# Optimization experiments

Hardware: AMD Instinct MI355X
Metric: run time of the kernel (lower is better)

The kernel has to match this reference:

```python
import jax, jax.numpy as jnp
import numpy as np

THEA = 0.5
DELTA = 1.5
IGNORE = 255
K = 19  # num classes (len(weights))
LOSS_WEIGHT = 1.0
MIN_PIXELS = 20.0  # class kept only if pixel count > 20
WEIGHTS = jnp.ones((K,), dtype=jnp.float32)
EPS = 1e-12


def setup_inputs() -> dict:
    key = jax.random.key(0)
    k1, k2 = jax.random.split(key)
    n, c, h, w = 4, 32, 512, 1024
    predict = jax.random.normal(k1, (n, c, h, w), dtype=jnp.float32)
    target = jax.random.randint(k2, (n, h, w), 0, K, dtype=jnp.int32)
    return {"predict": predict, "target": target}


def _loss(predict, target):
    n, c, h, w = predict.shape
    # (n,c,h,w) -> (n*h*w, c), matching predict.permute(0,2,3,1)
    feat = jnp.transpose(predict, (0, 2, 3, 1)).reshape(-1, c)
    seg = target.reshape(-1)
    valid_pix = seg != IGNORE
    seg = jnp.where(valid_pix, seg, K).astype(jnp.int32)  # ignored -> extra segment K
    ones = valid_pix.astype(feat.dtype)

    # per-class counts and means (segment reduce replaces the python class loop)
    counts = jax.ops.segment_sum(ones, seg, num_segments=K + 1)[:K]
    sums = jax.ops.segment_sum(feat * ones[:, None], seg, num_segments=K + 1)[:K]
    centers = sums / jnp.maximum(counts, 1.0)[:, None]  # [K, c]
    valid_cls = counts > MIN_PIXELS
    n_cls = jnp.maximum(jnp.sum(valid_cls.astype(feat.dtype)), 1.0)

    # ---- variance term: relu(||mean - x|| - thea)^2, normalized by #positives ----
    ctr_ext = jnp.concatenate([centers, jnp.zeros((1, c), centers.dtype)], axis=0)
    ctr_pix = ctr_ext[seg]  # gather per-pixel center
    res = jnp.sqrt(jnp.sum((ctr_pix - feat) ** 2, axis=1) + EPS)  # [n*h*w]
    r = jax.nn.relu(res - THEA) * ones
    sq = jax.ops.segment_sum(r * r, seg, num_segments=K + 1)[:K]
    pos = jax.ops.segment_sum((r > 0).astype(feat.dtype), seg, num_segments=K + 1)[:K]
    norml = jnp.maximum(jax.lax.stop_gradient(pos), 1.0)  # numpy count in original: no grad
    loss_var = jnp.sum(jnp.where(valid_cls, WEIGHTS * sq / norml, 0.0)) / n_cls

    # ---- pairwise center distance term ----
    diff = centers[:, None, :] - centers[None, :, :]  # [K, K, c]
    dist = jnp.sqrt(jnp.sum(diff * diff, axis=-1) + EPS)
    pair_mask = valid_cls[:, None] & valid_cls[None, :] & ~jnp.eye(K, dtype=bool)
    d = jax.nn.relu(2.0 * DELTA - dist)
    loss_dis = jnp.sum(jnp.where(pair_mask, d * d, 0.0)) / jnp.maximum(n_cls * (n_cls - 1.0), 1.0)

    # ---- regularization term ----
    loss_reg = jnp.sum(jnp.where(valid_cls, jnp.sqrt(jnp.sum(centers * centers, axis=1) + EPS), 0.0)) / n_cls

    return LOSS_WEIGHT * (loss_var + loss_dis + 0.001 * loss_reg)


def reference(predict, target):
    return _loss(predict, target)
```

## Files before the change

### kernel.cpp

```cpp
#include <hip/hip_runtime.h>


#define K_CLS 19
#define C_CH 32
#define HW_SHIFT 19
#define HW_SIZE (1 << HW_SHIFT)
#define EPSF 1e-12f
#define THEA_F 0.5f
#define TWO_DELTA 3.0f
#define MIN_PIX 20.0f

#define OFF_PSUM 0
#define OFF_PCNT 40960
#define OFF_RED  42240
#define OFF_VRED 42880
#define OFF_VPART 42944
#define WS_FLOATS (OFF_VPART + 1024 * 64)

typedef const unsigned int __attribute__((address_space(1)))* GP;
typedef unsigned int __attribute__((address_space(3)))* LP;

__device__ __forceinline__ void atomAddF(float* p, float v) {
  unsafeAtomicAdd(p, v);
}

__global__ __launch_bounds__(256) void k_accum(
    const float* __restrict__ pred, const int* __restrict__ tgt,
    float* __restrict__ ws)
{
  __shared__ float sA[4][K_CLS][64];
  __shared__ float sB[4][K_CLS][64];
  __shared__ float s_w[4][20];
  const int t = threadIdx.x;
  const int w = t >> 6;
  const int lane = t & 63;
  float* colA = &sA[w][0][lane];
  float* colB = &sB[w][0][lane];
#pragma unroll
  for (int k = 0; k < K_CLS; ++k) { colA[k << 6] = 0.f; colB[k << 6] = 0.f; }

  if (blockIdx.x < 2048) {
    const int plane = blockIdx.x >> 4;
    const int slab  = blockIdx.x & 15;
    const int n_idx = plane >> 5;
    const int ch    = plane & 31;
    const float* pbase = pred + (((size_t)plane) << HW_SHIFT) + ((size_t)slab << 15);
    const int*   tbase = tgt  + (((size_t)n_idx) << HW_SHIFT) + ((size_t)slab << 15);

    float4 vA = *reinterpret_cast<const float4*>(pbase + t * 4);
    int4   cA = *reinterpret_cast<const int4*>(tbase + t * 4);
#pragma unroll 1
    for (int it = 0; it < 32; ++it) {
      float4 vB; int4 cB;
      if (it + 1 < 32) {
        vB = *reinterpret_cast<const float4*>(pbase + (it + 1) * 1024 + t * 4);
        cB = *reinterpret_cast<const int4*>(tbase + (it + 1) * 1024 + t * 4);
      }
      const float x[4] = {vA.x, vA.y, vA.z, vA.w};
      const int   s[4] = {cA.x, cA.y, cA.z, cA.w};
      const int   k0 = min((unsigned)s[0], 18u), k1 = min((unsigned)s[1], 18u);
      const int   k2 = min((unsigned)s[2], 18u), k3 = min((unsigned)s[3], 18u);
      const float v0 = ((unsigned)s[0] < K_CLS) ? x[0] : 0.f;
      const float v1 = ((unsigned)s[1] < K_CLS) ? x[1] : 0.f;
      const float v2 = ((unsigned)s[2] < K_CLS) ? x[2] : 0.f;
      const float v3 = ((unsigned)s[3] < K_CLS) ? x[3] : 0.f;
      colA[k0 << 6] += v0;
      colB[k1 << 6] += v1;
      colA[k2 << 6] += v2;
      colB[k3 << 6] += v3;
      vA = vB; cA = cB;
    }

    float acc[K_CLS];
#pragma unroll
    for (int k = 0; k < K_CLS; ++k) acc[k] = colA[k << 6] + colB[k << 6];
#pragma unroll
    for (int k = 0; k < K_CLS; ++k) {
      float s = acc[k];
#pragma unroll
      for (int m = 1; m < 64; m <<= 1) s += __shfl_xor(s, m, 64);
      acc[k] = s;
    }
#pragma unroll
    for (int k = 0; k < K_CLS; ++k)
      if (lane == k) s_w[w][k] = acc[k];
    __syncthreads();
    if (t < K_CLS) {
      const int slot = n_idx * 16 + slab;
      ws[OFF_PSUM + ch * (64 * 20) + slot * 20 + t] =
          s_w[0][t] + s_w[1][t] + s_w[2][t] + s_w[3][t];
    }
  } else {
    const int idx = blockIdx.x - 2048;
    const int n_idx = idx >> 4;
    const int slab  = idx & 15;
    const int* tbase = tgt + (((size_t)n_idx) << HW_SHIFT) + ((size_t)slab << 15);

#pragma unroll 1
    for (int it = 0; it < 32; ++it) {
      const int4 c4 = *reinterpret_cast<const int4*>(tbase + it * 1024 + t * 4);
      const int s[4] = {c4.x, c4.y, c4.z, c4.w};
      const int k0 = min((unsigned)s[0], 18u), k1 = min((unsigned)s[1], 18u);
      const int k2 = min((unsigned)s[2], 18u), k3 = min((unsigned)s[3], 18u);
      colA[k0 << 6] += ((unsigned)s[0] < K_CLS) ? 1.f : 0.f;
      colB[k1 << 6] += ((unsigned)s[1] < K_CLS) ? 1.f : 0.f;
      colA[k2 << 6] += ((unsigned)s[2] < K_CLS) ? 1.f : 0.f;
      colB[k3 << 6] += ((unsigned)s[3] < K_CLS) ? 1.f : 0.f;
    }

    float acc[K_CLS];
#pragma unroll
    for (int k = 0; k < K_CLS; ++k) acc[k] = colA[k << 6] + colB[k << 6];
#pragma unroll
    for (int k = 0; k < K_CLS; ++k) {
      float s = acc[k];
#pragma unroll
      for (int m = 1; m < 64; m <<= 1) s += __shfl_xor(s, m, 64);
      acc[k] = s;
    }
#pragma unroll
    for (int k = 0; k < K_CLS; ++k)
      if (lane == k) s_w[w][k] = acc[k];
    __syncthreads();
    if (t < K_CLS) {
      const int slot = n_idx * 16 + slab;
      ws[OFF_PCNT + slot * 20 + t] = s_w[0][t] + s_w[1][t] + s_w[2][t] + s_w[3][t];
    }
  }
}

__global__ __launch_bounds__(64) void k_reduce(float* __restrict__ ws)
{
  const int o = blockIdx.x;
  const int lane = threadIdx.x;
  float a;
  if (o < C_CH * K_CLS) {
    const int ch = o / K_CLS, k = o - ch * K_CLS;
    a = ws[OFF_PSUM + ch * (64 * 20) + lane * 20 + k];
  } else {
    a = ws[OFF_PCNT + lane * 20 + (o - C_CH * K_CLS)];
  }
#pragma unroll
  for (int m = 1; m < 64; m <<= 1) a += __shfl_xor(a, m, 64);
  if (lane == 0) ws[OFF_RED + o] = a;
}

__global__ __launch_bounds__(256) void k_var(
    const float* __restrict__ pred, const int* __restrict__ tgt,
    float* __restrict__ ws)
{
  __shared__ float s_buf[4][2][C_CH][64];
  __shared__ int   s_cls[4][2][256];
  __shared__ float s_ctr[C_CH][K_CLS];
  __shared__ float s_sq[K_CLS];
  __shared__ float s_pos[K_CLS];

  const int t = threadIdx.x;
  const int w = t >> 6;
  const int lane = t & 63;

  for (int i = t; i < C_CH * K_CLS; i += 256) {
    const int k = i % K_CLS;
    (&s_ctr[0][0])[i] = ws[OFF_RED + i] / fmaxf(ws[OFF_RED + C_CH * K_CLS + k], 1.f);
  }
  if (t < K_CLS) { s_sq[t] = 0.f; s_pos[t] = 0.f; }
  __syncthreads();

  const size_t P0 = (size_t)blockIdx.x * 2048;
  const int n_idx = (int)(P0 >> HW_SHIFT);
  const int hw0 = (int)(P0 & (HW_SIZE - 1));
  const int qch = lane >> 4;
  const int qpx = (lane & 15) * 4;

#define STAGE(h, j)                                                           \
  {                                                                           \
    const int pw = hw0 + w * 512 + (j) * 64;                                  \
    _Pragma("unroll")                                                         \
    for (int q = 0; q < 8; ++q) {                                             \
      const int c = q * 4 + qch;                                              \
      const float* gp = pred + (((size_t)(n_idx * C_CH + c)) << HW_SHIFT)     \
                        + pw + qpx;                                           \
      __builtin_amdgcn_global_load_lds((GP)gp, (LP)&s_buf[w][h][0][0] + q * 256, \
                                       16, 0, 0);                             \
    }                                                                         \
    const int* gt = tgt + (((size_t)n_idx) << HW_SHIFT) + pw + qpx;           \
    __builtin_amdgcn_global_load_lds((GP)gt, (LP)&s_cls[w][h][0], 16, 0, 0);  \
  }

  float res8[8];
  int   cls8[8];

  STAGE(0, 0)
#pragma unroll 1
  for (int j = 0; j < 8; ++j) {
    const int h = j & 1;
    if (j < 7) {
      STAGE(h ^ 1, j + 1)
      asm volatile("s_waitcnt vmcnt(9)" ::: "memory");
    } else {
      asm volatile("s_waitcnt vmcnt(0)" ::: "memory");
    }
    __builtin_amdgcn_sched_barrier(0);

    const int ci = s_cls[w][h][lane];
    const bool vld = (unsigned)ci < K_CLS;
    const int sc = vld ? ci : 0;
    float d2 = 0.f;
#pragma unroll
    for (int c = 0; c < C_CH; ++c) {
      const float x = s_buf[w][h][c][lane];
      const float d = s_ctr[c][sc] - x;
      d2 = fmaf(d, d, d2);
    }
    res8[j] = d2;
    cls8[j] = vld ? ci : -1;
  }

#pragma unroll
  for (int j = 0; j < 8; ++j) {
    if (cls8[j] >= 0) {
      const float r = sqrtf(res8[j] + EPSF) - THEA_F;
      if (r > 0.f) { atomAddF(&s_sq[cls8[j]], r * r); atomAddF(&s_pos[cls8[j]], 1.f); }
    }
  }

  __syncthreads();
  if (t < K_CLS) {
    float* vp = ws + OFF_VPART + (size_t)blockIdx.x * 64;
    vp[t]         = s_sq[t];
    vp[K_CLS + t] = s_pos[t];
  }
#undef STAGE
}

__global__ __launch_bounds__(256) void k_vred(float* __restrict__ ws)
{
  const int o = blockIdx.x;
  const int t = threadIdx.x;
  float a = 0.f;
#pragma unroll
  for (int r = 0; r < 4; ++r)
    a += ws[OFF_VPART + (size_t)(t + r * 256) * 64 + o];
#pragma unroll
  for (int m = 1; m < 64; m <<= 1) a += __shfl_xor(a, m, 64);
  __shared__ float s[4];
  if ((t & 63) == 0) s[t >> 6] = a;
  __syncthreads();
  if (t == 0) ws[OFF_VRED + o] = s[0] + s[1] + s[2] + s[3];
}

__global__ __launch_bounds__(1024) void k_final(
    float* __restrict__ ws, float* __restrict__ out)
{
  __shared__ float s_ctr[C_CH * K_CLS];
  __shared__ float s_valid[K_CLS];
  __shared__ float s_red[3];
  __shared__ float s_ncls;
  const int t = threadIdx.x;
  if (t < 3) s_red[t] = 0.f;
  if (t < K_CLS) s_valid[t] = (ws[OFF_RED + C_CH * K_CLS + t] > MIN_PIX) ? 1.f : 0.f;
  for (int i = t; i < C_CH * K_CLS; i += 1024) {
    const int k = i % K_CLS;
    s_ctr[i] = ws[OFF_RED + i] / fmaxf(ws[OFF_RED + C_CH * K_CLS + k], 1.f);
  }
  __syncthreads();

  if (t == 0) {
    float n = 0.f;
    for (int k = 0; k < K_CLS; ++k) n += s_valid[k];
    s_ncls = fmaxf(n, 1.f);
  }
  if (t < K_CLS && s_valid[t] > 0.f) {
    const float sq  = ws[OFF_VRED + t];
    const float pos = ws[OFF_VRED + K_CLS + t];
    atomAddF(&s_red[0], sq / fmaxf(pos, 1.f));
    float nn = 0.f;
#pragma unroll
    for (int ch = 0; ch < C_CH; ++ch) {
      const float cv = s_ctr[ch * K_CLS + t];
      nn = fmaf(cv, cv, nn);
    }
    atomAddF(&s_red[2], sqrtf(nn + EPSF));
  }
  if (t < K_CLS * K_CLS) {
    const int a = t / K_CLS, b = t - (t / K_CLS) * K_CLS;
    if (a != b && s_valid[a] > 0.f && s_valid[b] > 0.f) {
      float dd = 0.f;
#pragma unroll
      for (int ch = 0; ch < C_CH; ++ch) {
        const float df = s_ctr[ch * K_CLS + a] - s_ctr[ch * K_CLS + b];
        dd = fmaf(df, df, dd);
      }
      const float dist = sqrtf(dd + EPSF);
      const float d = fmaxf(TWO_DELTA - dist, 0.f);
      if (d > 0.f) atomAddF(&s_red[1], d * d);
    }
  }
  __syncthreads();
  if (t == 0) {
    const float n = s_ncls;
    out[0] = s_red[0] / n
           + s_red[1] / fmaxf(n * (n - 1.f), 1.f)
           + 0.001f * s_red[2] / n;
  }
}

extern "C" void kernel_launch(void* const* d_in, const int* in_sizes, int n_in,
                              void* d_out, int out_size, void* d_ws, size_t ws_size,
                              hipStream_t stream) {
  const float* pred = (const float*)d_in[0];
  const int*   tgt  = (const int*)d_in[1];
  float* ws  = (float*)d_ws;
  float* out = (float*)d_out;
  const int P = in_sizes[1];
  const int nBlocksVar = P / 2048;

  k_accum <<<2048 + 64, 256, 0, stream>>>(pred, tgt, ws);
  k_reduce<<<C_CH * K_CLS + K_CLS, 64, 0, stream>>>(ws);
  k_var   <<<nBlocksVar, 256, 0, stream>>>(pred, tgt, ws);
  k_vred  <<<2 * K_CLS, 256, 0, stream>>>(ws);
  k_final <<<1, 1024, 0, stream>>>(ws, out);
}
```

Before: 449.6 us.

## Shrink LDS staging in variance kernel and replace shared atomics with register accumulators

The variance kernel now stages 16 channels per half-stage instead of 32, cutting its LDS footprint roughly in half so more blocks can be resident per CU. The wait counts are adjusted to match. Per-class sums and positive counts are kept in per-lane register arrays with select-based updates and reduced by wave shuffles, replacing shared-memory atomics. The accumulation kernel also drops its second per-class column buffer, accepting more LDS read-modify-write dependency in exchange for less LDS. The extra register arrays and the 19-way select per pixel add ALU work and register pressure.

```diff
diff --git a/kernel.cpp b/kernel.cpp
--- a/kernel.cpp
+++ b/kernel.cpp
@@ -29,15 +29,13 @@
     float* __restrict__ ws)
 {
   __shared__ float sA[4][K_CLS][64];
-  __shared__ float sB[4][K_CLS][64];
   __shared__ float s_w[4][20];
   const int t = threadIdx.x;
   const int w = t >> 6;
   const int lane = t & 63;
   float* colA = &sA[w][0][lane];
-  float* colB = &sB[w][0][lane];
-#pragma unroll
-  for (int k = 0; k < K_CLS; ++k) { colA[k << 6] = 0.f; colB[k << 6] = 0.f; }
+#pragma unroll
+  for (int k = 0; k < K_CLS; ++k) colA[k << 6] = 0.f;
 
   if (blockIdx.x < 2048) {
     const int plane = blockIdx.x >> 4;
@@ -65,15 +63,15 @@
       const float v2 = ((unsigned)s[2] < K_CLS) ? x[2] : 0.f;
       const float v3 = ((unsigned)s[3] < K_CLS) ? x[3] : 0.f;
       colA[k0 << 6] += v0;
-      colB[k1 << 6] += v1;
+      colA[k1 << 6] += v1;
       colA[k2 << 6] += v2;
-      colB[k3 << 6] += v3;
+      colA[k3 << 6] += v3;
       vA = vB; cA = cB;
     }
 
     float acc[K_CLS];
 #pragma unroll
-    for (int k = 0; k < K_CLS; ++k) acc[k] = colA[k << 6] + colB[k << 6];
+    for (int k = 0; k < K_CLS; ++k) acc[k] = colA[k << 6];
 #pragma unroll
     for (int k = 0; k < K_CLS; ++k) {
       float s = acc[k];
@@ -103,14 +101,14 @@
       const int k0 = min((unsigned)s[0], 18u), k1 = min((unsigned)s[1], 18u);
       const int k2 = min((unsigned)s[2], 18u), k3 = min((unsigned)s[3], 18u);
       colA[k0 << 6] += ((unsigned)s[0] < K_CLS) ? 1.f : 0.f;
-      colB[k1 << 6] += ((unsigned)s[1] < K_CLS) ? 1.f : 0.f;
+      colA[k1 << 6] += ((unsigned)s[1] < K_CLS) ? 1.f : 0.f;
       colA[k2 << 6] += ((unsigned)s[2] < K_CLS) ? 1.f : 0.f;
-      colB[k3 << 6] += ((unsigned)s[3] < K_CLS) ? 1.f : 0.f;
+      colA[k3 << 6] += ((unsigned)s[3] < K_CLS) ? 1.f : 0.f;
     }
 
     float acc[K_CLS];
 #pragma unroll
-    for (int k = 0; k < K_CLS; ++k) acc[k] = colA[k << 6] + colB[k << 6];
+    for (int k = 0; k < K_CLS; ++k) acc[k] = colA[k << 6];
 #pragma unroll
     for (int k = 0; k < K_CLS; ++k) {
       float s = acc[k];
@@ -149,11 +147,10 @@
     const float* __restrict__ pred, const int* __restrict__ tgt,
     float* __restrict__ ws)
 {
-  __shared__ float s_buf[4][2][C_CH][64];
-  __shared__ int   s_cls[4][2][256];
+  __shared__ float s_buf[4][2][16][64];
+  __shared__ int   s_cls[4][2][64];
   __shared__ float s_ctr[C_CH][K_CLS];
-  __shared__ float s_sq[K_CLS];
-  __shared__ float s_pos[K_CLS];
+  __shared__ float s_w[4][40];
 
   const int t = threadIdx.x;
   const int w = t >> 6;
@@ -163,74 +160,99 @@
     const int k = i % K_CLS;
     (&s_ctr[0][0])[i] = ws[OFF_RED + i] / fmaxf(ws[OFF_RED + C_CH * K_CLS + k], 1.f);
   }
-  if (t < K_CLS) { s_sq[t] = 0.f; s_pos[t] = 0.f; }
   __syncthreads();
 
   const size_t P0 = (size_t)blockIdx.x * 2048;
   const int n_idx = (int)(P0 >> HW_SHIFT);
   const int hw0 = (int)(P0 & (HW_SIZE - 1));
-  const int qch = lane >> 4;
-  const int qpx = (lane & 15) * 4;
-
-#define STAGE(h, j)                                                           \
+
+#define VSTAGE(s_)                                                            \
   {                                                                           \
-    const int pw = hw0 + w * 512 + (j) * 64;                                  \
+    const int p_ = (s_) & 1, pxw_ = (s_) >> 1;                                \
+    const int pw_ = hw0 + w * 512 + pxw_ * 64;                                \
+    const int cb_ = p_ * 16;                                                  \
     _Pragma("unroll")                                                         \
-    for (int q = 0; q < 8; ++q) {                                             \
-      const int c = q * 4 + qch;                                              \
-      const float* gp = pred + (((size_t)(n_idx * C_CH + c)) << HW_SHIFT)     \
-                        + pw + qpx;                                           \
-      __builtin_amdgcn_global_load_lds((GP)gp, (LP)&s_buf[w][h][0][0] + q * 256, \
+    for (int q = 0; q < 4; ++q) {                                             \
+      const int ch_ = cb_ + q * 4 + (lane >> 4);                              \
+      const float* gp = pred + (((size_t)(n_idx * C_CH + ch_)) << HW_SHIFT)   \
+                        + pw_ + (lane & 15) * 4;                              \
+      __builtin_amdgcn_global_load_lds((GP)gp, (LP)&s_buf[w][p_][q * 4][0],   \
                                        16, 0, 0);                             \
     }                                                                         \
-    const int* gt = tgt + (((size_t)n_idx) << HW_SHIFT) + pw + qpx;           \
-    __builtin_amdgcn_global_load_lds((GP)gt, (LP)&s_cls[w][h][0], 16, 0, 0);  \
-  }
-
-  float res8[8];
-  int   cls8[8];
-
-  STAGE(0, 0)
+    if (p_ == 0 && lane < 16) {                                               \
+      const int* gt = tgt + (((size_t)n_idx) << HW_SHIFT) + pw_ + lane * 4;   \
+      __builtin_amdgcn_global_load_lds((GP)gt, (LP)&s_cls[w][pxw_ & 1][0],    \
+                                       16, 0, 0);                             \
+    }                                                                         \
+  }
+
+  float acc_sq[K_CLS], acc_pos[K_CLS];
+#pragma unroll
+  for (int k = 0; k < K_CLS; ++k) { acc_sq[k] = 0.f; acc_pos[k] = 0.f; }
+
+  int  ci = 0, sc = 0;
+  bool vld = false;
+  float d2 = 0.f;
+
+  VSTAGE(0)
 #pragma unroll 1
-  for (int j = 0; j < 8; ++j) {
-    const int h = j & 1;
-    if (j < 7) {
-      STAGE(h ^ 1, j + 1)
-      asm volatile("s_waitcnt vmcnt(9)" ::: "memory");
+  for (int s = 0; s < 16; ++s) {
+    if (s < 15) {
+      VSTAGE(s + 1)
+      if (s & 1) asm volatile("s_waitcnt vmcnt(5)" ::: "memory");
+      else       asm volatile("s_waitcnt vmcnt(4)" ::: "memory");
     } else {
       asm volatile("s_waitcnt vmcnt(0)" ::: "memory");
     }
     __builtin_amdgcn_sched_barrier(0);
 
-    const int ci = s_cls[w][h][lane];
-    const bool vld = (unsigned)ci < K_CLS;
-    const int sc = vld ? ci : 0;
-    float d2 = 0.f;
-#pragma unroll
-    for (int c = 0; c < C_CH; ++c) {
-      const float x = s_buf[w][h][c][lane];
-      const float d = s_ctr[c][sc] - x;
+    const int p = s & 1, pxw = s >> 1, cb = p * 16;
+    if (p == 0) {
+      ci = s_cls[w][pxw & 1][lane];
+      vld = (unsigned)ci < K_CLS;
+      sc = vld ? ci : 0;
+      d2 = 0.f;
+    }
+#pragma unroll
+    for (int cc = 0; cc < 16; ++cc) {
+      const float x = s_buf[w][p][cc][lane];
+      const float d = s_ctr[cb + cc][sc] - x;
       d2 = fmaf(d, d, d2);
     }
-    res8[j] = d2;
-    cls8[j] = vld ? ci : -1;
-  }
-
-#pragma unroll
-  for (int j = 0; j < 8; ++j) {
-    if (cls8[j] >= 0) {
-      const float r = sqrtf(res8[j] + EPSF) - THEA_F;
-      if (r > 0.f) { atomAddF(&s_sq[cls8[j]], r * r); atomAddF(&s_pos[cls8[j]], 1.f); }
-    }
-  }
-
+    if (p == 1) {
+      const float r = sqrtf(d2 + EPSF) - THEA_F;
+      const bool act = vld && (r > 0.f);
+      const float rr = act ? r * r : 0.f;
+      const float pp = act ? 1.f : 0.f;
+#pragma unroll
+      for (int k = 0; k < K_CLS; ++k) {
+        const bool b = (sc == k);
+        acc_sq[k]  += b ? rr : 0.f;
+        acc_pos[k] += b ? pp : 0.f;
+      }
+    }
+  }
+#undef VSTAGE
+
+#pragma unroll
+  for (int k = 0; k < K_CLS; ++k) {
+    float a = acc_sq[k], b = acc_pos[k];
+#pragma unroll
+    for (int m = 1; m < 64; m <<= 1) {
+      a += __shfl_xor(a, m, 64);
+      b += __shfl_xor(b, m, 64);
+    }
+    acc_sq[k] = a; acc_pos[k] = b;
+  }
+#pragma unroll
+  for (int k = 0; k < K_CLS; ++k)
+    if (lane == k) { s_w[w][k] = acc_sq[k]; s_w[w][20 + k] = acc_pos[k]; }
   __syncthreads();
   if (t < K_CLS) {
     float* vp = ws + OFF_VPART + (size_t)blockIdx.x * 64;
-    vp[t]         = s_sq[t];
-    vp[K_CLS + t] = s_pos[t];
-  }
-#undef STAGE
+    vp[t]         = s_w[0][t] + s_w[1][t] + s_w[2][t] + s_w[3][t];
+    vp[K_CLS + t] = s_w[0][20 + t] + s_w[1][20 + t] + s_w[2][20 + t] + s_w[3][20 + t];
+  }
 }
 
 __global__ __launch_bounds__(256) void k_vred(float* __restrict__ ws)
```

New measurement: 436.0 us. 3.0% less time.

## Fuse accumulate, reduce and variance passes into one persistent kernel with grid barriers

Applied to the files above, without the earlier changes.

Merges the per-class sum/count accumulation, the partial reduction and the variance pass into a single 512-block kernel of 512 threads, synchronised by software grid barriers on a workspace counter that is cleared with a memset before launch. Counts are now computed inside the accumulation blocks instead of in separate blocks, and the variance pass uses a 3-slot async LDS ring with transposed center storage and vectorised center reads. The intent is to remove launch gaps and tail effects between the former kernels. In exchange it relies on all 512 blocks being co-resident, since the spin barrier deadlocks otherwise, and it uses fewer, larger blocks.

```diff
diff --git a/kernel.cpp b/kernel.cpp
--- a/kernel.cpp
+++ b/kernel.cpp
@@ -4,18 +4,18 @@
 #define K_CLS 19
 #define C_CH 32
 #define HW_SHIFT 19
-#define HW_SIZE (1 << HW_SHIFT)
 #define EPSF 1e-12f
 #define THEA_F 0.5f
 #define TWO_DELTA 3.0f
 #define MIN_PIX 20.0f
+#define NBLK 512
 
 #define OFF_PSUM 0
-#define OFF_PCNT 40960
-#define OFF_RED  42240
-#define OFF_VRED 42880
-#define OFF_VPART 42944
-#define WS_FLOATS (OFF_VPART + 1024 * 64)
+#define OFF_PCNT 10240
+#define OFF_RED  20480
+#define OFF_VRED 21120
+#define OFF_VPART 21184
+#define OFF_BAR  53952
 
 typedef const unsigned int __attribute__((address_space(1)))* GP;
 typedef unsigned int __attribute__((address_space(3)))* LP;
@@ -24,46 +24,99 @@
   unsafeAtomicAdd(p, v);
 }
 
-__global__ __launch_bounds__(256) void k_accum(
+#define SMEM_BYTES 78464
+
+__device__ __forceinline__ void grid_barrier(unsigned* bar, int phase) {
+  __syncthreads();
+  if (threadIdx.x == 0) {
+    __threadfence();
+    __hip_atomic_fetch_add(&bar[phase * 16 + (blockIdx.x & 15)], 1u,
+                           __ATOMIC_RELEASE, __HIP_MEMORY_SCOPE_AGENT);
+    unsigned sum = 0;
+    do {
+      __builtin_amdgcn_s_sleep(8);
+      sum = 0;
+      for (int i = 0; i < 16; ++i)
+        sum += __hip_atomic_load(&bar[phase * 16 + i],
+                                 __ATOMIC_ACQUIRE, __HIP_MEMORY_SCOPE_AGENT);
+    } while (sum < NBLK);
+  }
+  __syncthreads();
+}
+
+__global__ __launch_bounds__(512, 4) void k_fused(
     const float* __restrict__ pred, const int* __restrict__ tgt,
-    float* __restrict__ ws)
+    float* __restrict__ ws, unsigned* __restrict__ bar)
 {
-  __shared__ float sA[4][K_CLS][64];
-  __shared__ float sB[4][K_CLS][64];
-  __shared__ float s_w[4][20];
+  __shared__ __align__(16) char smem[SMEM_BYTES];
+  float* smf = (float*)smem;
   const int t = threadIdx.x;
   const int w = t >> 6;
   const int lane = t & 63;
-  float* colA = &sA[w][0][lane];
-  float* colB = &sB[w][0][lane];
-#pragma unroll
-  for (int k = 0; k < K_CLS; ++k) { colA[k << 6] = 0.f; colB[k << 6] = 0.f; }
-
-  if (blockIdx.x < 2048) {
-    const int plane = blockIdx.x >> 4;
-    const int slab  = blockIdx.x & 15;
+  const int bid = blockIdx.x;
+
+  {
+    const int plane = bid >> 2;
+    const int slab  = bid & 3;
     const int n_idx = plane >> 5;
     const int ch    = plane & 31;
-    const float* pbase = pred + (((size_t)plane) << HW_SHIFT) + ((size_t)slab << 15);
-    const int*   tbase = tgt  + (((size_t)n_idx) << HW_SHIFT) + ((size_t)slab << 15);
+    const float* pbase = pred + (((size_t)plane) << HW_SHIFT) + ((size_t)slab << 17);
+    const int*   tbase = tgt  + (((size_t)n_idx) << HW_SHIFT) + ((size_t)slab << 17);
+
+    float* colA = smf + w * (K_CLS * 64) + lane;
+    float* colB = smf + 9728 + w * (K_CLS * 64) + lane;
+#pragma unroll
+    for (int k = 0; k < K_CLS; ++k) { colA[k << 6] = 0.f; colB[k << 6] = 0.f; }
+
+    {
+      const int* cb = tbase + ch * 4096;
+      const int4 c0 = *reinterpret_cast<const int4*>(cb + t * 8);
+      const int4 c1 = *reinterpret_cast<const int4*>(cb + t * 8 + 4);
+      const int cs[8] = {c0.x, c0.y, c0.z, c0.w, c1.x, c1.y, c1.z, c1.w};
+      float accc[K_CLS];
+#pragma unroll
+      for (int k = 0; k < K_CLS; ++k) accc[k] = 0.f;
+#pragma unroll
+      for (int j = 0; j < 8; ++j) {
+#pragma unroll
+        for (int k = 0; k < K_CLS; ++k) accc[k] += (cs[j] == k) ? 1.f : 0.f;
+      }
+#pragma unroll
+      for (int k = 0; k < K_CLS; ++k) {
+        float s = accc[k];
+#pragma unroll
+        for (int m = 1; m < 64; m <<= 1) s += __shfl_xor(s, m, 64);
+        accc[k] = s;
+      }
+      float* s_w = smf + 19456;
+#pragma unroll
+      for (int k = 0; k < K_CLS; ++k)
+        if (lane == k) s_w[w * 20 + k] = accc[k];
+      __syncthreads();
+      if (t < K_CLS) {
+        float a = 0.f;
+#pragma unroll
+        for (int ww = 0; ww < 8; ++ww) a += s_w[ww * 20 + t];
+        ws[OFF_PCNT + bid * 20 + t] = a;
+      }
+      __syncthreads();
+    }
 
     float4 vA = *reinterpret_cast<const float4*>(pbase + t * 4);
     int4   cA = *reinterpret_cast<const int4*>(tbase + t * 4);
 #pragma unroll 1
-    for (int it = 0; it < 32; ++it) {
+    for (int it = 0; it < 64; ++it) {
       float4 vB; int4 cB;
-      if (it + 1 < 32) {
-        vB = *reinterpret_cast<const float4*>(pbase + (it + 1) * 1024 + t * 4);
-        cB = *reinterpret_cast<const int4*>(tbase + (it + 1) * 1024 + t * 4);
-      }
-      const float x[4] = {vA.x, vA.y, vA.z, vA.w};
-      const int   s[4] = {cA.x, cA.y, cA.z, cA.w};
-      const int   k0 = min((unsigned)s[0], 18u), k1 = min((unsigned)s[1], 18u);
-      const int   k2 = min((unsigned)s[2], 18u), k3 = min((unsigned)s[3], 18u);
-      const float v0 = ((unsigned)s[0] < K_CLS) ? x[0] : 0.f;
-      const float v1 = ((unsigned)s[1] < K_CLS) ? x[1] : 0.f;
-      const float v2 = ((unsigned)s[2] < K_CLS) ? x[2] : 0.f;
-      const float v3 = ((unsigned)s[3] < K_CLS) ? x[3] : 0.f;
+      if (it + 1 < 64) {
+        vB = *reinterpret_cast<const float4*>(pbase + (it + 1) * 2048 + t * 4);
+        cB = *reinterpret_cast<const int4*>(tbase + (it + 1) * 2048 + t * 4);
+      }
+      const int k0 = min((unsigned)cA.x, 18u), k1 = min((unsigned)cA.y, 18u);
+      const int k2 = min((unsigned)cA.z, 18u), k3 = min((unsigned)cA.w, 18u);
+      const float v0 = ((unsigned)cA.x < K_CLS) ? vA.x : 0.f;
+      const float v1 = ((unsigned)cA.y < K_CLS) ? vA.y : 0.f;
+      const float v2 = ((unsigned)cA.z < K_CLS) ? vA.z : 0.f;
+      const float v3 = ((unsigned)cA.w < K_CLS) ? vA.w : 0.f;
       colA[k0 << 6] += v0;
       colB[k1 << 6] += v1;
       colA[k2 << 6] += v2;
@@ -81,156 +134,141 @@
       for (int m = 1; m < 64; m <<= 1) s += __shfl_xor(s, m, 64);
       acc[k] = s;
     }
-#pragma unroll
-    for (int k = 0; k < K_CLS; ++k)
-      if (lane == k) s_w[w][k] = acc[k];
+    {
+      float* s_w = smf + 19456;
+#pragma unroll
+      for (int k = 0; k < K_CLS; ++k)
+        if (lane == k) s_w[w * 20 + k] = acc[k];
+      __syncthreads();
+      if (t < K_CLS) {
+        float a = 0.f;
+#pragma unroll
+        for (int ww = 0; ww < 8; ++ww) a += s_w[ww * 20 + t];
+        ws[OFF_PSUM + ch * 320 + (n_idx * 4 + slab) * 20 + t] = a;
+      }
+    }
+  }
+
+  grid_barrier(bar, 0);
+
+  {
+    const int ch = bid / K_CLS, k = bid - ch * K_CLS;
+    if (t < 16) {
+      float a = ws[OFF_PSUM + ch * 320 + t * 20 + k];
+      a += __shfl_xor(a, 1, 64);
+      a += __shfl_xor(a, 2, 64);
+      a += __shfl_xor(a, 4, 64);
+      a += __shfl_xor(a, 8, 64);
+      if (t == 0) ws[OFF_RED + bid] = a;
+    }
+  }
+  if (bid < 96) {
+    const int j = bid + 512;
+    const int ch = j / K_CLS, k = j - ch * K_CLS;
+    if (t < 16) {
+      float a = ws[OFF_PSUM + ch * 320 + t * 20 + k];
+      a += __shfl_xor(a, 1, 64);
+      a += __shfl_xor(a, 2, 64);
+      a += __shfl_xor(a, 4, 64);
+      a += __shfl_xor(a, 8, 64);
+      if (t == 0) ws[OFF_RED + j] = a;
+    }
+  } else if (bid < 99) {
+    const int k = (bid - 96) * 8 + w;
+    if (k < K_CLS) {
+      float a = 0.f;
+#pragma unroll
+      for (int m = 0; m < 8; ++m)
+        a += ws[OFF_PCNT + (lane + m * 64) * 20 + k];
+#pragma unroll
+      for (int m2 = 1; m2 < 64; m2 <<= 1) a += __shfl_xor(a, m2, 64);
+      if (lane == 0) ws[OFF_RED + 608 + k] = a;
+    }
+  }
+
+  grid_barrier(bar, 1);
+
+  {
+    float* ctrT = smf + 12288;
+    float* bins = smf + 12976;
+    for (int i = t; i < C_CH * K_CLS; i += 512) {
+      const int c = i / K_CLS, s = i - c * K_CLS;
+      ctrT[s * 36 + c] = ws[OFF_RED + i] / fmaxf(ws[OFF_RED + 608 + s], 1.f);
+    }
+    if (t < 320) bins[t] = 0.f;
     __syncthreads();
-    if (t < K_CLS) {
-      const int slot = n_idx * 16 + slab;
-      ws[OFF_PSUM + ch * (64 * 20) + slot * 20 + t] =
-          s_w[0][t] + s_w[1][t] + s_w[2][t] + s_w[3][t];
-    }
-  } else {
-    const int idx = blockIdx.x - 2048;
-    const int n_idx = idx >> 4;
-    const int slab  = idx & 15;
-    const int* tbase = tgt + (((size_t)n_idx) << HW_SHIFT) + ((size_t)slab << 15);
-
-#pragma unroll 1
-    for (int it = 0; it < 32; ++it) {
-      const int4 c4 = *reinterpret_cast<const int4*>(tbase + it * 1024 + t * 4);
-      const int s[4] = {c4.x, c4.y, c4.z, c4.w};
-      const int k0 = min((unsigned)s[0], 18u), k1 = min((unsigned)s[1], 18u);
-      const int k2 = min((unsigned)s[2], 18u), k3 = min((unsigned)s[3], 18u);
-      colA[k0 << 6] += ((unsigned)s[0] < K_CLS) ? 1.f : 0.f;
-      colB[k1 << 6] += ((unsigned)s[1] < K_CLS) ? 1.f : 0.f;
-      colA[k2 << 6] += ((unsigned)s[2] < K_CLS) ? 1.f : 0.f;
-      colB[k3 << 6] += ((unsigned)s[3] < K_CLS) ? 1.f : 0.f;
-    }
-
-    float acc[K_CLS];
-#pragma unroll
-    for (int k = 0; k < K_CLS; ++k) acc[k] = colA[k << 6] + colB[k << 6];
-#pragma unroll
-    for (int k = 0; k < K_CLS; ++k) {
-      float s = acc[k];
-#pragma unroll
-      for (int m = 1; m < 64; m <<= 1) s += __shfl_xor(s, m, 64);
-      acc[k] = s;
-    }
-#pragma unroll
-    for (int k = 0; k < K_CLS; ++k)
-      if (lane == k) s_w[w][k] = acc[k];
+
+    const size_t pxb = (size_t)bid * 4096;
+    const int n_idx = (int)(pxb >> HW_SHIFT);
+    const int hw0 = (int)(pxb & ((1 << HW_SHIFT) - 1)) + w * 512;
+    const int nC = n_idx * C_CH;
+
+    int cls[8];
+#pragma unroll
+    for (int win = 0; win < 8; ++win)
+      cls[win] = tgt[((size_t)n_idx << HW_SHIFT) + hw0 + win * 64 + lane];
+
+#define ISSUE(sidx)                                                           \
+    { const int win_ = (sidx) >> 2, q_ = (sidx) & 3, ring_ = (sidx) % 3;      \
+      const int pw_ = hw0 + win_ * 64;                                        \
+      _Pragma("unroll")                                                       \
+      for (int j = 0; j < 2; ++j) {                                           \
+        const int ch_ = q_ * 8 + j * 4 + (lane >> 4);                         \
+        const float* gp = pred + (((size_t)(nC + ch_)) << HW_SHIFT)           \
+                          + pw_ + (lane & 15) * 4;                            \
+        __builtin_amdgcn_global_load_lds((GP)gp,                              \
+            (LP)(smem + (w * 6144 + ring_ * 2048 + j * 1024)), 16, 0, 0);     \
+      } }
+
+    ISSUE(0)
+    ISSUE(1)
+
+#pragma unroll
+    for (int win = 0; win < 8; ++win) {
+      const int c0 = cls[win];
+      const bool vld = (unsigned)c0 < K_CLS;
+      const int sc = vld ? c0 : 0;
+      float d2 = 0.f;
+#pragma unroll
+      for (int q = 0; q < 4; ++q) {
+        const int sidx = win * 4 + q;
+        if (sidx + 2 <= 31) ISSUE(sidx + 2)
+        if (sidx <= 29)      { asm volatile("s_waitcnt vmcnt(4)" ::: "memory"); }
+        else if (sidx == 30) { asm volatile("s_waitcnt vmcnt(2)" ::: "memory"); }
+        else                 { asm volatile("s_waitcnt vmcnt(0)" ::: "memory"); }
+        __builtin_amdgcn_sched_barrier(0);
+        const int ring = sidx % 3;
+        const float* stg = smf + w * 1536 + ring * 512;
+        const float4 g0 = *reinterpret_cast<const float4*>(&ctrT[sc * 36 + q * 8]);
+        const float4 g1 = *reinterpret_cast<const float4*>(&ctrT[sc * 36 + q * 8 + 4]);
+        const float x0 = stg[0 * 64 + lane], x1 = stg[1 * 64 + lane];
+        const float x2 = stg[2 * 64 + lane], x3 = stg[3 * 64 + lane];
+        const float x4 = stg[4 * 64 + lane], x5 = stg[5 * 64 + lane];
+        const float x6 = stg[6 * 64 + lane], x7 = stg[7 * 64 + lane];
+        const float e0 = g0.x - x0, e1 = g0.y - x1, e2 = g0.z - x2, e3 = g0.w - x3;
+        const float e4 = g1.x - x4, e5 = g1.y - x5, e6 = g1.z - x6, e7 = g1.w - x7;
+        d2 = fmaf(e0, e0, d2); d2 = fmaf(e1, e1, d2);
+        d2 = fmaf(e2, e2, d2); d2 = fmaf(e3, e3, d2);
+        d2 = fmaf(e4, e4, d2); d2 = fmaf(e5, e5, d2);
+        d2 = fmaf(e6, e6, d2); d2 = fmaf(e7, e7, d2);
+      }
+      const float r = sqrtf(d2 + EPSF) - THEA_F;
+      if (vld && r > 0.f) {
+        atomAddF(&bins[w * 40 + sc], r * r);
+        atomAddF(&bins[w * 40 + 20 + sc], 1.f);
+      }
+    }
+#undef ISSUE
+
     __syncthreads();
-    if (t < K_CLS) {
-      const int slot = n_idx * 16 + slab;
-      ws[OFF_PCNT + slot * 20 + t] = s_w[0][t] + s_w[1][t] + s_w[2][t] + s_w[3][t];
-    }
-  }
-}
-
-__global__ __launch_bounds__(64) void k_reduce(float* __restrict__ ws)
-{
-  const int o = blockIdx.x;
-  const int lane = threadIdx.x;
-  float a;
-  if (o < C_CH * K_CLS) {
-    const int ch = o / K_CLS, k = o - ch * K_CLS;
-    a = ws[OFF_PSUM + ch * (64 * 20) + lane * 20 + k];
-  } else {
-    a = ws[OFF_PCNT + lane * 20 + (o - C_CH * K_CLS)];
-  }
-#pragma unroll
-  for (int m = 1; m < 64; m <<= 1) a += __shfl_xor(a, m, 64);
-  if (lane == 0) ws[OFF_RED + o] = a;
-}
-
-__global__ __launch_bounds__(256) void k_var(
-    const float* __restrict__ pred, const int* __restrict__ tgt,
-    float* __restrict__ ws)
-{
-  __shared__ float s_buf[4][2][C_CH][64];
-  __shared__ int   s_cls[4][2][256];
-  __shared__ float s_ctr[C_CH][K_CLS];
-  __shared__ float s_sq[K_CLS];
-  __shared__ float s_pos[K_CLS];
-
-  const int t = threadIdx.x;
-  const int w = t >> 6;
-  const int lane = t & 63;
-
-  for (int i = t; i < C_CH * K_CLS; i += 256) {
-    const int k = i % K_CLS;
-    (&s_ctr[0][0])[i] = ws[OFF_RED + i] / fmaxf(ws[OFF_RED + C_CH * K_CLS + k], 1.f);
-  }
-  if (t < K_CLS) { s_sq[t] = 0.f; s_pos[t] = 0.f; }
-  __syncthreads();
-
-  const size_t P0 = (size_t)blockIdx.x * 2048;
-  const int n_idx = (int)(P0 >> HW_SHIFT);
-  const int hw0 = (int)(P0 & (HW_SIZE - 1));
-  const int qch = lane >> 4;
-  const int qpx = (lane & 15) * 4;
-
-#define STAGE(h, j)                                                           \
-  {                                                                           \
-    const int pw = hw0 + w * 512 + (j) * 64;                                  \
-    _Pragma("unroll")                                                         \
-    for (int q = 0; q < 8; ++q) {                                             \
-      const int c = q * 4 + qch;                                              \
-      const float* gp = pred + (((size_t)(n_idx * C_CH + c)) << HW_SHIFT)     \
-                        + pw + qpx;                                           \
-      __builtin_amdgcn_global_load_lds((GP)gp, (LP)&s_buf[w][h][0][0] + q * 256, \
-                                       16, 0, 0);                             \
-    }                                                                         \
-    const int* gt = tgt + (((size_t)n_idx) << HW_SHIFT) + pw + qpx;           \
-    __builtin_amdgcn_global_load_lds((GP)gt, (LP)&s_cls[w][h][0], 16, 0, 0);  \
-  }
-
-  float res8[8];
-  int   cls8[8];
-
-  STAGE(0, 0)
-#pragma unroll 1
-  for (int j = 0; j < 8; ++j) {
-    const int h = j & 1;
-    if (j < 7) {
-      STAGE(h ^ 1, j + 1)
-      asm volatile("s_waitcnt vmcnt(9)" ::: "memory");
-    } else {
-      asm volatile("s_waitcnt vmcnt(0)" ::: "memory");
-    }
-    __builtin_amdgcn_sched_barrier(0);
-
-    const int ci = s_cls[w][h][lane];
-    const bool vld = (unsigned)ci < K_CLS;
-    const int sc = vld ? ci : 0;
-    float d2 = 0.f;
-#pragma unroll
-    for (int c = 0; c < C_CH; ++c) {
-      const float x = s_buf[w][h][c][lane];
-      const float d = s_ctr[c][sc] - x;
-      d2 = fmaf(d, d, d2);
-    }
-    res8[j] = d2;
-    cls8[j] = vld ? ci : -1;
-  }
-
-#pragma unroll
-  for (int j = 0; j < 8; ++j) {
-    if (cls8[j] >= 0) {
-      const float r = sqrtf(res8[j] + EPSF) - THEA_F;
-      if (r > 0.f) { atomAddF(&s_sq[cls8[j]], r * r); atomAddF(&s_pos[cls8[j]], 1.f); }
-    }
-  }
-
-  __syncthreads();
-  if (t < K_CLS) {
-    float* vp = ws + OFF_VPART + (size_t)blockIdx.x * 64;
-    vp[t]         = s_sq[t];
-    vp[K_CLS + t] = s_pos[t];
-  }
-#undef STAGE
+    if (t < 2 * K_CLS) {
+      const int slot = (t < K_CLS) ? t : (20 + (t - K_CLS));
+      float a = 0.f;
+#pragma unroll
+      for (int ww = 0; ww < 8; ++ww) a += bins[ww * 40 + slot];
+      ws[OFF_VPART + (size_t)bid * 64 + t] = a;
+    }
+  }
 }
 
 __global__ __launch_bounds__(256) void k_vred(float* __restrict__ ws)
@@ -239,7 +277,7 @@
   const int t = threadIdx.x;
   float a = 0.f;
 #pragma unroll
-  for (int r = 0; r < 4; ++r)
+  for (int r = 0; r < 2; ++r)
     a += ws[OFF_VPART + (size_t)(t + r * 256) * 64 + o];
 #pragma unroll
   for (int m = 1; m < 64; m <<= 1) a += __shfl_xor(a, m, 64);
@@ -312,12 +350,10 @@
   const int*   tgt  = (const int*)d_in[1];
   float* ws  = (float*)d_ws;
   float* out = (float*)d_out;
-  const int P = in_sizes[1];
-  const int nBlocksVar = P / 2048;
-
-  k_accum <<<2048 + 64, 256, 0, stream>>>(pred, tgt, ws);
-  k_reduce<<<C_CH * K_CLS + K_CLS, 64, 0, stream>>>(ws);
-  k_var   <<<nBlocksVar, 256, 0, stream>>>(pred, tgt, ws);
-  k_vred  <<<2 * K_CLS, 256, 0, stream>>>(ws);
-  k_final <<<1, 1024, 0, stream>>>(ws, out);
-}
+
+  hipMemsetAsync((char*)d_ws + OFF_BAR * 4, 0, 32 * 4, stream);
+  k_fused<<<NBLK, 512, 0, stream>>>(pred, tgt, ws,
+                                    (unsigned*)((float*)d_ws + OFF_BAR));
+  k_vred <<<2 * K_CLS, 256, 0, stream>>>(ws);
+  k_final<<<1, 1024, 0, stream>>>(ws, out);
+}
```

Result: slower. 744.2 us (+65.5%).
